# Optimization experiments

Measured on AMD Instinct MI355X. Metric: run time of the kernel, lower is better.

## Reference

```python
import jax, jax.numpy as jnp
import numpy as np

# dims: batch, samples, agents, obs_dim, action_dim, hidden
B, S, N, D, A, H = 512, 64, 8, 64, 16, 256
IN_DIM = (D + A) * N  # 640


def mish(x):
    return x * jnp.tanh(jax.nn.softplus(x))


def setup_inputs() -> dict:
    key = jax.random.key(0)
    ks = jax.random.split(key, 9)
    u = lambda k, shape, fan_in: jax.random.uniform(
        k, shape, jnp.float32, -1.0 / np.sqrt(fan_in), 1.0 / np.sqrt(fan_in))
    return {
        "state": jax.random.normal(ks[0], (B, N, D), jnp.float32),
        "action": jax.random.normal(ks[1], (B, N, A), jnp.float32),
        "W1": u(ks[2], (IN_DIM, H), IN_DIM),
        "b1": u(ks[3], (H,), IN_DIM),
        "W2": u(ks[4], (H, H), H),
        "b2": u(ks[5], (H,), H),
        "W3": u(ks[6], (H, 1), H),
        "b3": u(ks[7], (1,), H),
        # random grand-coalition permutations of the N agents, per (batch, sample)
        "perm": jnp.argsort(jax.random.uniform(ks[8], (B, S, N)), axis=-1).astype(jnp.int32),
    }


def reference(state, action, W1, b1, W2, b2, W3, b3, perm):
    # subcoalition mask [B,S,N,N]: torch builds one-hot(perm) @ tril(ones),
    # i.e. mask[b,s,i,j] = 1 iff j <= perm[b,s,i]
    subcoal = (jnp.arange(N) <= perm[..., None]).astype(state.dtype)
    # gathered actions in coalition order [B,S,N,A]: act_g[b,s,j] = action[b, perm[b,s,j]]
    act_g = action[jnp.arange(B)[:, None, None], perm]
    # masked subcoalition actions [B,S,N,N,A] -> [B,S,N,N*A]
    act = (act_g[:, :, None, :, :] * subcoal[..., None]).reshape(B, S, N, N * A)
    # flattened global obs broadcast over (sample, agent) axes [B,S,N,N*D]
    obs = jnp.broadcast_to(state.reshape(B, 1, 1, N * D), (B, S, N, N * D))
    x = jnp.concatenate([obs, act], axis=-1)  # [B,S,N,IN_DIM]
    # per-agent loop in torch uses shared q1 weights -> single batched MLP
    h = mish(x @ W1 + b1)
    h = mish(h @ W2 + b2)
    q = h @ W3 + b3                   # [B,S,N,1]
    q1 = q.mean(axis=1).squeeze(-1)   # mean over samples -> [B,N]
    return (q1, q1)
```

## Files before the change

kernel.cpp:

```cpp
#include <hip/hip_runtime.h>

typedef unsigned short ushort_t;
typedef _Float16 half_t;
typedef __attribute__((ext_vector_type(2))) _Float16 half2_t;
typedef __attribute__((ext_vector_type(8))) _Float16 half8_t;
typedef __attribute__((ext_vector_type(2))) __fp16 fp16x2;
typedef __attribute__((ext_vector_type(2))) float fx2;
typedef __attribute__((ext_vector_type(4))) float floatx4;

#define LOG2E 1.4426950408889634f
#define LN2   0.6931471805599453f

__device__ __forceinline__ float exp2_(float x) {
#if __has_builtin(__builtin_amdgcn_exp2f)
    return __builtin_amdgcn_exp2f(x);
#else
    return exp2f(x);
#endif
}

__device__ __forceinline__ half2_t cvt_pk_f16(float a, float b) {
    auto r = __builtin_amdgcn_cvt_pkrtz(a, b);
    return __builtin_bit_cast(half2_t, r);
}

__device__ __forceinline__ float fdot2_(half2_t a, half2_t b) {
#if __has_builtin(__builtin_amdgcn_fdot2)
    return __builtin_amdgcn_fdot2(__builtin_bit_cast(fp16x2, a),
                                  __builtin_bit_cast(fp16x2, b), 0.0f, false);
#else
    return (float)a.x * (float)b.x + (float)a.y * (float)b.y;
#endif
}

__device__ __forceinline__ fx2 mish2(fx2 t0) {
    fx2 one = {1.0f, 1.0f};
    fx2 m2  = {-2.0f, -2.0f};
    fx2 u   = {exp2_(t0.x), exp2_(t0.y)};
    fx2 s   = u + one;
    fx2 wv  = __builtin_elementwise_fma(s, s, one);
    fx2 rr  = {__builtin_amdgcn_rcpf(wv.x), __builtin_amdgcn_rcpf(wv.y)};
    fx2 v   = __builtin_elementwise_fma(rr, m2, one);
    return t0 * v;
}

__device__ __forceinline__ float dpp_sum16(float v) {
    int x = __float_as_int(v);
    v += __int_as_float(__builtin_amdgcn_update_dpp(0, x, 0xB1, 0xF, 0xF, true));
    x = __float_as_int(v);
    v += __int_as_float(__builtin_amdgcn_update_dpp(0, x, 0x4E, 0xF, 0xF, true));
    x = __float_as_int(v);
    v += __int_as_float(__builtin_amdgcn_update_dpp(0, x, 0x124, 0xF, 0xF, true));
    x = __float_as_int(v);
    v += __int_as_float(__builtin_amdgcn_update_dpp(0, x, 0x128, 0xF, 0xF, true));
    return v;
}

__global__ __launch_bounds__(256) void prep_kernel(
        const float* __restrict__ state,
        const float* __restrict__ action,
        const float* __restrict__ W1,
        const float* __restrict__ W2,
        float* __restrict__ obsWp,
        half_t* __restrict__ actW,
        half_t* __restrict__ W2T,
        float* __restrict__ out) {
    int bid = blockIdx.x;
    int t = threadIdx.x;
    if (bid < 512) {
        int bg = bid >> 3;
        int kc = bid & 7;
        int bs = bg * 8;
        const float* w1p = W1 + (size_t)(kc * 64) * 256 + t;
        const float* stp = state + (size_t)bs * 512 + kc * 64;
        float acc[8];
#pragma unroll
        for (int bb = 0; bb < 8; ++bb) acc[bb] = 0.f;
#pragma unroll 4
        for (int f = 0; f < 64; ++f) {
            float w = w1p[f * 256];
#pragma unroll
            for (int bb = 0; bb < 8; ++bb)
                acc[bb] = fmaf(stp[bb * 512 + f], w, acc[bb]);
        }
#pragma unroll
        for (int bb = 0; bb < 8; ++bb)
            obsWp[(size_t)kc * 131072 + (bs + bb) * 256 + t] = acc[bb];
    } else if (bid < 1536) {
        int idx = bid - 512;
        int j = idx & 7;
        int b0 = (idx >> 3) * 4;
        const float* W1a = W1 + (size_t)(512 + j * 16) * 256;
        float wv[16];
#pragma unroll
        for (int a = 0; a < 16; ++a) wv[a] = W1a[a * 256 + t];
#pragma unroll
        for (int bb = 0; bb < 4; ++bb) {
            int b = b0 + bb;
            const float* acp = action + (size_t)b * 128;
            float acc[8];
#pragma unroll
            for (int n = 0; n < 8; ++n) acc[n] = 0.f;
#pragma unroll
            for (int a = 0; a < 16; ++a) {
#pragma unroll
                for (int n = 0; n < 8; ++n)
                    acc[n] = fmaf(acp[n * 16 + a], wv[a], acc[n]);
            }
#pragma unroll
            for (int n = 0; n < 8; ++n)
                actW[(((size_t)b * 8 + n) * 8 + j) * 256 + t] = (half_t)(acc[n] * LOG2E);
        }
    } else {
        int blk = bid - 1536;
        if (blk < 16) {
            out[blk * 512 + t] = 0.0f;
            out[blk * 512 + 256 + t] = 0.0f;
        }
        int n = blk * 8 + (t >> 5);
        int klo = t & 31;
#pragma unroll
        for (int kk = 0; kk < 8; ++kk) {
            int k = kk * 32 + klo;
            W2T[n * 256 + k] = (half_t)W2[k * 256 + n];
        }
    }
}

#define CHUNK_US 528
#define UNROLL_ _Pragma("unroll")

#define KPHASE(EPF, BUILDF, RD, DST, ACC, ACCP, QH, AV)                        \
  {                                                                            \
    UNROLL_ for (int mt = 0; mt < 4; ++mt) {                                   \
      UNROLL_ for (int nt = 0; nt < 2; ++nt)                                   \
        ACC[mt][nt] = (floatx4){0.f, 0.f, 0.f, 0.f};                           \
    }                                                                          \
    fx2 r01_ = {ob.x, ob.y};                                                   \
    fx2 r23_ = {ob.z, ob.w};                                                   \
    UNROLL_ for (int ks = 0; ks < 8; ++ks) {                                   \
      half8_t afr[4];                                                          \
      UNROLL_ for (int mt = 0; mt < 4; ++mt)                                   \
        afr[mt] = *reinterpret_cast<const half8_t*>((RD) + (mt * 8 + ks) * CHUNK_US); \
      half8_t bfr0 = (ks == 0) ? bpre[0] : (ks == 1) ? bpre[2]                 \
                   : *reinterpret_cast<const half8_t*>(w2base + 0 * 4096 + ks * 32); \
      half8_t bfr1 = (ks == 0) ? bpre[1] : (ks == 1) ? bpre[3]                 \
                   : *reinterpret_cast<const half8_t*>(w2base + 1 * 4096 + ks * 32); \
      UNROLL_ for (int mt = 0; mt < 4; ++mt) {                                 \
        ACC[mt][0] = __builtin_amdgcn_mfma_f32_16x16x32_f16(afr[mt], bfr0, ACC[mt][0], 0, 0, 0); \
        ACC[mt][1] = __builtin_amdgcn_mfma_f32_16x16x32_f16(afr[mt], bfr1, ACC[mt][1], 0, 0, 0); \
      }                                                                        \
      if (BUILDF) {                                                            \
        half2_t a0_ = __builtin_bit_cast(half2_t, AV[ks].x);                   \
        half2_t a1_ = __builtin_bit_cast(half2_t, AV[ks].y);                   \
        r01_ += (fx2){(float)a0_.x, (float)a0_.y};                             \
        r23_ += (fx2){(float)a1_.x, (float)a1_.y};                             \
        fx2 h01_ = mish2(r01_);                                                \
        fx2 h23_ = mish2(r23_);                                                \
        int row_ = w * 8 + ks;                                                 \
        int mt2_ = row_ >> 4, lr_ = row_ & 15;                                 \
        int lrs_ = (lr_ + qq) & 15;                                            \
        uint2 pk_ = make_uint2(                                                \
            __builtin_bit_cast(unsigned, cvt_pk_f16(h01_.x, h01_.y)),          \
            __builtin_bit_cast(unsigned, cvt_pk_f16(h23_.x, h23_.y)));         \
        *reinterpret_cast<uint2*>((DST) + mt2_ * 8 * CHUNK_US + lrs_ * 8) = pk_; \
      }                                                                        \
      if (EPF) {                                                               \
        UNROLL_ for (int v = 0; v < 2; ++v) {                                  \
          int idx_ = ks * 2 + v;                                               \
          int mt_ = idx_ >> 2, r_ = idx_ & 3;                                  \
          fx2 t2_ = {ACCP[mt_][0][r_], ACCP[mt_][1][r_]};                      \
          t2_ += b2p;                                                          \
          fx2 hh_ = mish2(t2_);                                                \
          float part_ = fdot2_(cvt_pk_f16(hh_.x, hh_.y), w3p);                 \
          float sr_ = dpp_sum16(part_);                                        \
          if (lo == 0) qpart[QH][w][mt_ * 16 + q * 4 + r_] = sr_;              \
        }                                                                      \
      }                                                                        \
    }                                                                          \
  }

#define GATHER(AV, HALF)                                                       \
  UNROLL_ for (int j = 0; j < 8; ++j) {                                        \
    int p_ = perm_s[((HALF) * 8 + w) * 8 + j];                                 \
    AV[j] = *reinterpret_cast<const uint2*>(actg + (p_ * 8 + j) * 256);        \
  }

__global__ __launch_bounds__(512, 4) void main_kernel(
        const float* __restrict__ obsWp, const half_t* __restrict__ actW,
        const half_t* __restrict__ W2T, const int* __restrict__ perm,
        const float* __restrict__ b1, const float* __restrict__ b2,
        const float* __restrict__ W3, const float* __restrict__ b3,
        float* __restrict__ out) {
    __shared__ __align__(16) ushort_t h1[2][32 * CHUNK_US];
    __shared__ __align__(16) float obsb[256];
    __shared__ int perm_s[256];
    __shared__ float qpart[4][8][64];

    int t = threadIdx.x;
    int bid = blockIdx.x;
    int b = (bid & 7) * 64 + ((bid >> 3) & 63);
    int sgp = bid >> 9;
    int s0 = sgp * 32;

    int w = t >> 6;
    int L = t & 63;
    int lo = L & 15;
    int q = L >> 4;

    const half_t* w2base = W2T + ((size_t)(w * 32 + lo)) * 256 + q * 8;
    half8_t bpre[4];
    bpre[0] = *reinterpret_cast<const half8_t*>(w2base + 0 * 4096 + 0 * 32);
    bpre[1] = *reinterpret_cast<const half8_t*>(w2base + 1 * 4096 + 0 * 32);
    bpre[2] = *reinterpret_cast<const half8_t*>(w2base + 0 * 4096 + 1 * 32);
    bpre[3] = *reinterpret_cast<const half8_t*>(w2base + 1 * 4096 + 1 * 32);

    int col0 = w * 32 + lo;
    int col1 = col0 + 16;
    fx2 b2p = {b2[col0] * LOG2E, b2[col1] * LOG2E};
    half2_t w3p = cvt_pk_f16(W3[col0] * LN2, W3[col1] * LN2);

    const int* prow = perm + ((size_t)b * 64 + s0 + w) * 8;
    int4 pa0 = *reinterpret_cast<const int4*>(prow);
    int4 pa1 = *reinterpret_cast<const int4*>(prow + 4);

    if (t < 256) {
        float s = b1[t];
#pragma unroll
        for (int c = 0; c < 8; ++c) s += obsWp[(size_t)c * 131072 + b * 256 + t];
        obsb[t] = s * LOG2E;
    } else {
        perm_s[t - 256] = perm[((size_t)b * 64 + s0) * 8 + (t - 256)];
    }

    int g = L >> 1;
    int ksg = g >> 2;
    int qq = g & 3;
    int halfsel = L & 1;
    const half_t* actg = actW + (size_t)b * 64 * 256 + L * 4;
    int dstoff = qq * 128 + halfsel * 4 + ksg * CHUNK_US;

    int pj0[8] = {pa0.x, pa0.y, pa0.z, pa0.w, pa1.x, pa1.y, pa1.z, pa1.w};
    uint2 av_a[8];
#pragma unroll
    for (int j = 0; j < 8; ++j)
        av_a[j] = *reinterpret_cast<const uint2*>(actg + (pj0[j] * 8 + j) * 256);

    int phys = (q << 4) | ((lo + q) & 15);
    ushort_t* dst0 = h1[0] + dstoff;
    ushort_t* dst1 = h1[1] + dstoff;
    const ushort_t* rd0 = h1[0] + phys * 8;
    const ushort_t* rd1 = h1[1] + phys * 8;

    __syncthreads();

    float4 ob = *reinterpret_cast<const float4*>(obsb + L * 4);

    {
        fx2 r01 = {ob.x, ob.y};
        fx2 r23 = {ob.z, ob.w};
#pragma unroll
        for (int j = 0; j < 8; ++j) {
            half2_t a0 = __builtin_bit_cast(half2_t, av_a[j].x);
            half2_t a1 = __builtin_bit_cast(half2_t, av_a[j].y);
            r01 += (fx2){(float)a0.x, (float)a0.y};
            r23 += (fx2){(float)a1.x, (float)a1.y};
            fx2 h01 = mish2(r01);
            fx2 h23 = mish2(r23);
            int row = w * 8 + j;
            int mt2 = row >> 4, lr = row & 15;
            int lrs = (lr + qq) & 15;
            uint2 pk = make_uint2(__builtin_bit_cast(unsigned, cvt_pk_f16(h01.x, h01.y)),
                                  __builtin_bit_cast(unsigned, cvt_pk_f16(h23.x, h23.y)));
            *reinterpret_cast<uint2*>(dst0 + mt2 * 8 * CHUNK_US + lrs * 8) = pk;
        }
    }

    uint2 av_b[8];
    GATHER(av_b, 1)

    __syncthreads();

    floatx4 acc_a[4][2], acc_b[4][2];

    KPHASE(false, true, rd0, dst1, acc_a, acc_a, 0, av_b)

    GATHER(av_a, 2)

    __syncthreads();

    KPHASE(true, true, rd1, dst0, acc_b, acc_a, 0, av_a)

    GATHER(av_b, 3)

    __syncthreads();

    KPHASE(true, true, rd0, dst1, acc_a, acc_b, 1, av_b)

    __syncthreads();

    KPHASE(true, false, rd1, dst1, acc_b, acc_a, 2, av_b)

#pragma unroll
    for (int idx = 0; idx < 16; ++idx) {
        int mt = idx >> 2, r = idx & 3;
        fx2 t2 = {acc_b[mt][0][r], acc_b[mt][1][r]};
        t2 += b2p;
        fx2 hh = mish2(t2);
        float part = fdot2_(cvt_pk_f16(hh.x, hh.y), w3p);
        float s = dpp_sum16(part);
        if (lo == 0) qpart[3][w][mt * 16 + q * 4 + r] = s;
    }
    __syncthreads();

    if (t < 32) {
        int h = t >> 3, i = t & 7;
        float p = 0.f;
#pragma unroll
        for (int sl = 0; sl < 8; ++sl) {
            int k = perm_s[(h * 8 + sl) * 8 + i];
            int row = sl * 8 + k;
            float qv = b3[0];
#pragma unroll
            for (int ww = 0; ww < 8; ++ww) qv += qpart[h][ww][row];
            p += qv;
        }
        p *= (1.0f / 64.0f);
        atomicAdd(&out[b * 8 + i], p);
        atomicAdd(&out[4096 + b * 8 + i], p);
    }
}

extern "C" void kernel_launch(void* const* d_in, const int* in_sizes, int n_in,
                              void* d_out, int out_size, void* d_ws, size_t ws_size,
                              hipStream_t stream) {
    const float* state  = (const float*)d_in[0];
    const float* action = (const float*)d_in[1];
    const float* W1     = (const float*)d_in[2];
    const float* b1     = (const float*)d_in[3];
    const float* W2     = (const float*)d_in[4];
    const float* b2     = (const float*)d_in[5];
    const float* W3     = (const float*)d_in[6];
    const float* b3     = (const float*)d_in[7];
    const int*   perm   = (const int*)d_in[8];
    float* out = (float*)d_out;

    char* ws = (char*)d_ws;
    float*  obsWp = (float*)ws;
    half_t* actW  = (half_t*)(ws + 4194304);
    half_t* W2T   = (half_t*)(ws + 4194304 + 16777216);

    prep_kernel<<<1568, 256, 0, stream>>>(state, action, W1, W2, obsWp, actW, W2T, out);
    main_kernel<<<1024, 512, 0, stream>>>(obsWp, actW, W2T, perm, b1, b2, W3, b3, out);
}
```

Baseline: 198.6 us.

## Halve per-block sample tile to raise occupancy and split agent rows across waves

After: 262.0 us. +31.9%, slower.

```diff
diff --git a/kernel.cpp b/kernel.cpp
--- a/kernel.cpp
+++ b/kernel.cpp
@@ -130,97 +130,101 @@
 #define CHUNK_US 528
 #define UNROLL_ _Pragma("unroll")
 
-#define KPHASE(EPF, BUILDF, RD, DST, ACC, ACCP, QH, AV)                        \
-  {                                                                            \
-    UNROLL_ for (int mt = 0; mt < 4; ++mt) {                                   \
+#define GATHERQ(AV, PR, QTR)                                                   \
+  { int s_ = (QTR) * 4 + siq;                                                  \
+    UNROLL_ for (int k = 0; k < 4; ++k) {                                      \
+      int p_ = perm_s[s_ * 8 + nb + k];                                        \
+      AV[k] = *reinterpret_cast<const uint2*>(actg + (p_ * 8 + nb + k) * 256); \
+    }                                                                          \
+    if (nb) {                                                                  \
+      UNROLL_ for (int k = 0; k < 4; ++k) {                                    \
+        int p_ = perm_s[s_ * 8 + k];                                           \
+        PR[k] = *reinterpret_cast<const uint2*>(actg + (p_ * 8 + k) * 256);    \
+      }                                                                        \
+    } }
+
+#define KPHASE(RD, ACC, EPF, ACCP, QH, BUILDF, AV, PR, DSTP)                   \
+  { UNROLL_ for (int mt = 0; mt < 2; ++mt) {                                   \
       UNROLL_ for (int nt = 0; nt < 2; ++nt)                                   \
         ACC[mt][nt] = (floatx4){0.f, 0.f, 0.f, 0.f};                           \
     }                                                                          \
     fx2 r01_ = {ob.x, ob.y};                                                   \
     fx2 r23_ = {ob.z, ob.w};                                                   \
+    if ((BUILDF) && nb) {                                                      \
+      UNROLL_ for (int k = 0; k < 4; ++k) {                                    \
+        half2_t a0_ = __builtin_bit_cast(half2_t, PR[k].x);                    \
+        half2_t a1_ = __builtin_bit_cast(half2_t, PR[k].y);                    \
+        r01_ += (fx2){(float)a0_.x, (float)a0_.y};                             \
+        r23_ += (fx2){(float)a1_.x, (float)a1_.y};                             \
+      }                                                                        \
+    }                                                                          \
     UNROLL_ for (int ks = 0; ks < 8; ++ks) {                                   \
-      half8_t afr[4];                                                          \
-      UNROLL_ for (int mt = 0; mt < 4; ++mt)                                   \
-        afr[mt] = *reinterpret_cast<const half8_t*>((RD) + (mt * 8 + ks) * CHUNK_US); \
-      half8_t bfr0 = (ks == 0) ? bpre[0] : (ks == 1) ? bpre[2]                 \
-                   : *reinterpret_cast<const half8_t*>(w2base + 0 * 4096 + ks * 32); \
-      half8_t bfr1 = (ks == 0) ? bpre[1] : (ks == 1) ? bpre[3]                 \
-                   : *reinterpret_cast<const half8_t*>(w2base + 1 * 4096 + ks * 32); \
-      UNROLL_ for (int mt = 0; mt < 4; ++mt) {                                 \
-        ACC[mt][0] = __builtin_amdgcn_mfma_f32_16x16x32_f16(afr[mt], bfr0, ACC[mt][0], 0, 0, 0); \
-        ACC[mt][1] = __builtin_amdgcn_mfma_f32_16x16x32_f16(afr[mt], bfr1, ACC[mt][1], 0, 0, 0); \
-      }                                                                        \
-      if (BUILDF) {                                                            \
-        half2_t a0_ = __builtin_bit_cast(half2_t, AV[ks].x);                   \
-        half2_t a1_ = __builtin_bit_cast(half2_t, AV[ks].y);                   \
+      half8_t afr0_ = *reinterpret_cast<const half8_t*>((RD) + (0 * 8 + ks) * CHUNK_US); \
+      half8_t afr1_ = *reinterpret_cast<const half8_t*>((RD) + (1 * 8 + ks) * CHUNK_US); \
+      half8_t bfr0_ = *reinterpret_cast<const half8_t*>(w2base + 0 * 4096 + ks * 32); \
+      half8_t bfr1_ = *reinterpret_cast<const half8_t*>(w2base + 1 * 4096 + ks * 32); \
+      ACC[0][0] = __builtin_amdgcn_mfma_f32_16x16x32_f16(afr0_, bfr0_, ACC[0][0], 0, 0, 0); \
+      ACC[0][1] = __builtin_amdgcn_mfma_f32_16x16x32_f16(afr0_, bfr1_, ACC[0][1], 0, 0, 0); \
+      ACC[1][0] = __builtin_amdgcn_mfma_f32_16x16x32_f16(afr1_, bfr0_, ACC[1][0], 0, 0, 0); \
+      ACC[1][1] = __builtin_amdgcn_mfma_f32_16x16x32_f16(afr1_, bfr1_, ACC[1][1], 0, 0, 0); \
+      if ((BUILDF) && !(ks & 1)) {                                             \
+        int jp_ = ks >> 1;                                                     \
+        half2_t a0_ = __builtin_bit_cast(half2_t, AV[jp_].x);                  \
+        half2_t a1_ = __builtin_bit_cast(half2_t, AV[jp_].y);                  \
         r01_ += (fx2){(float)a0_.x, (float)a0_.y};                             \
         r23_ += (fx2){(float)a1_.x, (float)a1_.y};                             \
         fx2 h01_ = mish2(r01_);                                                \
         fx2 h23_ = mish2(r23_);                                                \
-        int row_ = w * 8 + ks;                                                 \
+        int row_ = siq * 8 + nb + jp_;                                         \
         int mt2_ = row_ >> 4, lr_ = row_ & 15;                                 \
-        int lrs_ = (lr_ + qq) & 15;                                            \
         uint2 pk_ = make_uint2(                                                \
             __builtin_bit_cast(unsigned, cvt_pk_f16(h01_.x, h01_.y)),          \
             __builtin_bit_cast(unsigned, cvt_pk_f16(h23_.x, h23_.y)));         \
-        *reinterpret_cast<uint2*>((DST) + mt2_ * 8 * CHUNK_US + lrs_ * 8) = pk_; \
+        *reinterpret_cast<uint2*>((DSTP) + mt2_ * 8 * CHUNK_US + lr_ * 8) = pk_; \
       }                                                                        \
       if (EPF) {                                                               \
-        UNROLL_ for (int v = 0; v < 2; ++v) {                                  \
-          int idx_ = ks * 2 + v;                                               \
-          int mt_ = idx_ >> 2, r_ = idx_ & 3;                                  \
-          fx2 t2_ = {ACCP[mt_][0][r_], ACCP[mt_][1][r_]};                      \
-          t2_ += b2p;                                                          \
-          fx2 hh_ = mish2(t2_);                                                \
-          float part_ = fdot2_(cvt_pk_f16(hh_.x, hh_.y), w3p);                 \
-          float sr_ = dpp_sum16(part_);                                        \
-          if (lo == 0) qpart[QH][w][mt_ * 16 + q * 4 + r_] = sr_;              \
-        }                                                                      \
+        int mt_ = ks >> 2, r_ = ks & 3;                                        \
+        fx2 t2_ = {ACCP[mt_][0][r_], ACCP[mt_][1][r_]};                        \
+        t2_ += b2p;                                                            \
+        fx2 hh_ = mish2(t2_);                                                  \
+        float part_ = fdot2_(cvt_pk_f16(hh_.x, hh_.y), w3p);                   \
+        float sr_ = dpp_sum16(part_);                                          \
+        if (lo == 0) qpart[QH][w][mt_ * 16 + q * 4 + r_] = sr_;                \
       }                                                                        \
-    }                                                                          \
-  }
-
-#define GATHER(AV, HALF)                                                       \
-  UNROLL_ for (int j = 0; j < 8; ++j) {                                        \
-    int p_ = perm_s[((HALF) * 8 + w) * 8 + j];                                 \
-    AV[j] = *reinterpret_cast<const uint2*>(actg + (p_ * 8 + j) * 256);        \
-  }
-
-__global__ __launch_bounds__(512, 4) void main_kernel(
+    } }
+
+__global__ __launch_bounds__(512, 6) void main_kernel(
         const float* __restrict__ obsWp, const half_t* __restrict__ actW,
         const half_t* __restrict__ W2T, const int* __restrict__ perm,
         const float* __restrict__ b1, const float* __restrict__ b2,
         const float* __restrict__ W3, const float* __restrict__ b3,
         float* __restrict__ out) {
-    __shared__ __align__(16) ushort_t h1[2][32 * CHUNK_US];
+    __shared__ __align__(16) ushort_t h1[2][16 * CHUNK_US];
     __shared__ __align__(16) float obsb[256];
-    __shared__ int perm_s[256];
-    __shared__ float qpart[4][8][64];
+    __shared__ int perm_s[128];
+    __shared__ float qpart[4][8][32];
 
     int t = threadIdx.x;
     int bid = blockIdx.x;
     int b = (bid & 7) * 64 + ((bid >> 3) & 63);
     int sgp = bid >> 9;
-    int s0 = sgp * 32;
+    int s0 = sgp * 16;
 
     int w = t >> 6;
     int L = t & 63;
     int lo = L & 15;
     int q = L >> 4;
+    int siq = w & 3;
+    int nb = (w >> 2) * 4;
 
     const half_t* w2base = W2T + ((size_t)(w * 32 + lo)) * 256 + q * 8;
-    half8_t bpre[4];
-    bpre[0] = *reinterpret_cast<const half8_t*>(w2base + 0 * 4096 + 0 * 32);
-    bpre[1] = *reinterpret_cast<const half8_t*>(w2base + 1 * 4096 + 0 * 32);
-    bpre[2] = *reinterpret_cast<const half8_t*>(w2base + 0 * 4096 + 1 * 32);
-    bpre[3] = *reinterpret_cast<const half8_t*>(w2base + 1 * 4096 + 1 * 32);
 
     int col0 = w * 32 + lo;
     int col1 = col0 + 16;
     fx2 b2p = {b2[col0] * LOG2E, b2[col1] * LOG2E};
     half2_t w3p = cvt_pk_f16(W3[col0] * LN2, W3[col1] * LN2);
 
-    const int* prow = perm + ((size_t)b * 64 + s0 + w) * 8;
+    const int* prow = perm + ((size_t)b * 64 + s0 + siq) * 8;
     int4 pa0 = *reinterpret_cast<const int4*>(prow);
     int4 pa1 = *reinterpret_cast<const int4*>(prow + 4);
 
@@ -229,7 +233,7 @@
 #pragma unroll
         for (int c = 0; c < 8; ++c) s += obsWp[(size_t)c * 131072 + b * 256 + t];
         obsb[t] = s * LOG2E;
-    } else {
+    } else if (t < 384) {
         perm_s[t - 256] = perm[((size_t)b * 64 + s0) * 8 + (t - 256)];
     }
 
@@ -240,17 +244,25 @@
     const half_t* actg = actW + (size_t)b * 64 * 256 + L * 4;
     int dstoff = qq * 128 + halfsel * 4 + ksg * CHUNK_US;
 
-    int pj0[8] = {pa0.x, pa0.y, pa0.z, pa0.w, pa1.x, pa1.y, pa1.z, pa1.w};
-    uint2 av_a[8];
-#pragma unroll
-    for (int j = 0; j < 8; ++j)
-        av_a[j] = *reinterpret_cast<const uint2*>(actg + (pj0[j] * 8 + j) * 256);
-
-    int phys = (q << 4) | ((lo + q) & 15);
+    int pjb0 = nb ? pa1.x : pa0.x, pjb1 = nb ? pa1.y : pa0.y;
+    int pjb2 = nb ? pa1.z : pa0.z, pjb3 = nb ? pa1.w : pa0.w;
+    uint2 av_a[4], pr_a[4];
+    uint2 av_b[4], pr_b[4];
+    av_a[0] = *reinterpret_cast<const uint2*>(actg + (pjb0 * 8 + nb + 0) * 256);
+    av_a[1] = *reinterpret_cast<const uint2*>(actg + (pjb1 * 8 + nb + 1) * 256);
+    av_a[2] = *reinterpret_cast<const uint2*>(actg + (pjb2 * 8 + nb + 2) * 256);
+    av_a[3] = *reinterpret_cast<const uint2*>(actg + (pjb3 * 8 + nb + 3) * 256);
+    if (nb) {
+        pr_a[0] = *reinterpret_cast<const uint2*>(actg + (pa0.x * 8 + 0) * 256);
+        pr_a[1] = *reinterpret_cast<const uint2*>(actg + (pa0.y * 8 + 1) * 256);
+        pr_a[2] = *reinterpret_cast<const uint2*>(actg + (pa0.z * 8 + 2) * 256);
+        pr_a[3] = *reinterpret_cast<const uint2*>(actg + (pa0.w * 8 + 3) * 256);
+    }
+
     ushort_t* dst0 = h1[0] + dstoff;
     ushort_t* dst1 = h1[1] + dstoff;
-    const ushort_t* rd0 = h1[0] + phys * 8;
-    const ushort_t* rd1 = h1[1] + phys * 8;
+    const ushort_t* rd0 = h1[0] + L * 8;
+    const ushort_t* rd1 = h1[1] + L * 8;
 
     __syncthreads();
 
@@ -259,52 +271,59 @@
     {
         fx2 r01 = {ob.x, ob.y};
         fx2 r23 = {ob.z, ob.w};
-#pragma unroll
-        for (int j = 0; j < 8; ++j) {
+        if (nb) {
+#pragma unroll
+            for (int k = 0; k < 4; ++k) {
+                half2_t a0 = __builtin_bit_cast(half2_t, pr_a[k].x);
+                half2_t a1 = __builtin_bit_cast(half2_t, pr_a[k].y);
+                r01 += (fx2){(float)a0.x, (float)a0.y};
+                r23 += (fx2){(float)a1.x, (float)a1.y};
+            }
+        }
+#pragma unroll
+        for (int j = 0; j < 4; ++j) {
             half2_t a0 = __builtin_bit_cast(half2_t, av_a[j].x);
             half2_t a1 = __builtin_bit_cast(half2_t, av_a[j].y);
             r01 += (fx2){(float)a0.x, (float)a0.y};
             r23 += (fx2){(float)a1.x, (float)a1.y};
             fx2 h01 = mish2(r01);
             fx2 h23 = mish2(r23);
-            int row = w * 8 + j;
+            int row = siq * 8 + nb + j;
             int mt2 = row >> 4, lr = row & 15;
-            int lrs = (lr + qq) & 15;
             uint2 pk = make_uint2(__builtin_bit_cast(unsigned, cvt_pk_f16(h01.x, h01.y)),
                                   __builtin_bit_cast(unsigned, cvt_pk_f16(h23.x, h23.y)));
-            *reinterpret_cast<uint2*>(dst0 + mt2 * 8 * CHUNK_US + lrs * 8) = pk;
-        }
-    }
-
-    uint2 av_b[8];
-    GATHER(av_b, 1)
-
-    __syncthreads();
-
-    floatx4 acc_a[4][2], acc_b[4][2];
-
-    KPHASE(false, true, rd0, dst1, acc_a, acc_a, 0, av_b)
-
-    GATHER(av_a, 2)
-
-    __syncthreads();
-
-    KPHASE(true, true, rd1, dst0, acc_b, acc_a, 0, av_a)
-
-    GATHER(av_b, 3)
-
-    __syncthreads();
-
-    KPHASE(true, true, rd0, dst1, acc_a, acc_b, 1, av_b)
-
-    __syncthreads();
-
-    KPHASE(true, false, rd1, dst1, acc_b, acc_a, 2, av_b)
-
-#pragma unroll
-    for (int idx = 0; idx < 16; ++idx) {
+            *reinterpret_cast<uint2*>(dst0 + mt2 * 8 * CHUNK_US + lr * 8) = pk;
+        }
+    }
+
+    GATHERQ(av_b, pr_b, 1)
+
+    __syncthreads();
+
+    floatx4 accA[2][2], accB[2][2];
+
+    KPHASE(rd0, accA, false, accA, 0, true, av_b, pr_b, dst1)
+
+    GATHERQ(av_a, pr_a, 2)
+
+    __syncthreads();
+
+    KPHASE(rd1, accB, true, accA, 0, true, av_a, pr_a, dst0)
+
+    GATHERQ(av_b, pr_b, 3)
+
+    __syncthreads();
+
+    KPHASE(rd0, accA, true, accB, 1, true, av_b, pr_b, dst1)
+
+    __syncthreads();
+
+    KPHASE(rd1, accB, true, accA, 2, false, av_b, pr_b, dst1)
+
+#pragma unroll
+    for (int idx = 0; idx < 8; ++idx) {
         int mt = idx >> 2, r = idx & 3;
-        fx2 t2 = {acc_b[mt][0][r], acc_b[mt][1][r]};
+        fx2 t2 = {accB[mt][0][r], accB[mt][1][r]};
         t2 += b2p;
         fx2 hh = mish2(t2);
         float part = fdot2_(cvt_pk_f16(hh.x, hh.y), w3p);
@@ -313,16 +332,17 @@
     }
     __syncthreads();
 
-    if (t < 32) {
-        int h = t >> 3, i = t & 7;
+    if (t < 16) {
+        int i = t & 7, gg = t >> 3;
         float p = 0.f;
 #pragma unroll
         for (int sl = 0; sl < 8; ++sl) {
-            int k = perm_s[(h * 8 + sl) * 8 + i];
-            int row = sl * 8 + k;
+            int s = gg * 8 + sl;
+            int k = perm_s[s * 8 + i];
+            int row = (s & 3) * 8 + k;
             float qv = b3[0];
 #pragma unroll
-            for (int ww = 0; ww < 8; ++ww) qv += qpart[h][ww][row];
+            for (int ww = 0; ww < 8; ++ww) qv += qpart[s >> 2][ww][row];
             p += qv;
         }
         p *= (1.0f / 64.0f);
@@ -351,5 +371,5 @@
     half_t* W2T   = (half_t*)(ws + 4194304 + 16777216);
 
     prep_kernel<<<1568, 256, 0, stream>>>(state, action, W1, W2, obsWp, actW, W2T, out);
-    main_kernel<<<1024, 512, 0, stream>>>(obsWp, actW, W2T, perm, b1, b2, W3, b3, out);
-}
+    main_kernel<<<2048, 512, 0, stream>>>(obsWp, actW, W2T, perm, b1, b2, W3, b3, out);
+}
```
